# Kernel optimization log

Hardware: AMD Instinct MI355X
Metric: run time of the kernel (lower is better)

## Reference

```python
import jax, jax.numpy as jnp
import numpy as np

TAU = 1.0        # gumbel-softmax temperature
H = 8            # n_heads
RD = 32          # routing_dim


def setup_inputs() -> dict:
    key = jax.random.key(0)
    k1, k2, k3, k4, k5 = jax.random.split(key, 5)
    B, T, C = 2, 2048, 1024
    x = jax.random.normal(k1, (B, T, C), dtype=jnp.float32)
    # base adjacency [H,T,T]; keep diagonal free so each causal row has a finite logit
    base_mask = jax.random.randint(k2, (H, T, T), 0, 2).astype(bool)
    base_mask = base_mask & ~jnp.eye(T, dtype=bool)[None]
    # pre-sampled standard Gumbel noise (matches F.gumbel_softmax internals)
    u = jax.random.uniform(k3, (B, H, T, T), dtype=jnp.float32, minval=1e-9, maxval=1.0)
    gumbel = -jnp.log(-jnp.log(u))
    scale = 1.0 / np.sqrt(C).astype(np.float32)
    Wq = jax.random.normal(k4, (C, H * RD), dtype=jnp.float32) * scale
    Wk = jax.random.normal(k5, (C, H * RD), dtype=jnp.float32) * scale
    return {"x": x, "base_mask": base_mask, "gumbel": gumbel, "Wq": Wq, "Wk": Wk}


def reference(x, base_mask, gumbel, Wq, Wk):
    B, T, C = x.shape
    # routing projections -> [B,T,H,RD]
    sq = (x @ Wq).reshape(B, T, H, RD)
    sk = (x @ Wk).reshape(B, T, H, RD)
    # pairwise edge scores [B,H,T,T]
    scores = jnp.einsum("bihd,bjhd->bhij", sq, sk) / np.sqrt(RD).astype(np.float32)
    # causal mask (j > i) OR already-connected base edges -> -inf
    causal = jnp.triu(jnp.ones((T, T), dtype=bool), 1)
    mask = causal[None, None] | base_mask[None]
    scores = jnp.where(mask, -jnp.inf, scores)
    # gumbel-softmax (training path, hard=False): softmax((logits + g) / tau)
    return jax.nn.softmax((scores + gumbel) / TAU, axis=-1)
```

## Files before the change

kernel.cpp:

```cpp
#include <hip/hip_runtime.h>
#include <hip/hip_bf16.h>
#include <math.h>

#define TT    2048
#define HH    8
#define RDIM  32
#define BB    2

typedef float  f4  __attribute__((ext_vector_type(4)));
typedef int    i4  __attribute__((ext_vector_type(4)));
typedef uint   u2  __attribute__((ext_vector_type(2)));
typedef uint   u4  __attribute__((ext_vector_type(4)));
typedef short  s8v __attribute__((ext_vector_type(8)));

__device__ __forceinline__ uint rnd16(float x) {
    return (__float_as_uint(x) + 0x8000u) >> 16;
}

union v8cast { u4 u; s8v s; };

__global__ __launch_bounds__(256) void wt_prep(
    const float* __restrict__ Wq,
    const float* __restrict__ Wk,
    ushort* __restrict__ Wt)
{
    __shared__ float T[64][68];
    const int k0 = blockIdx.x * 64;
    const int n0 = blockIdx.y * 64;
    const float* W = (n0 < 256) ? Wq : Wk;
    const int nloc = n0 & 255;
    const int tid = threadIdx.x;

    #pragma unroll
    for (int r = 0; r < 4; ++r) {
        int kl  = (tid >> 4) + r * 16;
        int nl4 = (tid & 15) * 4;
        f4 v = *(const f4*)&W[(size_t)(k0 + kl) * 256 + nloc + nl4];
        T[nl4 + 0][kl] = v.x;
        T[nl4 + 1][kl] = v.y;
        T[nl4 + 2][kl] = v.z;
        T[nl4 + 3][kl] = v.w;
    }
    __syncthreads();

    const int nl = tid >> 2;
    const int kq = (tid & 3) * 16;
    u4 o0, o1;
    #pragma unroll
    for (int j = 0; j < 4; ++j) {
        uint lo = rnd16(T[nl][kq + 2 * j]);
        uint hi = rnd16(T[nl][kq + 2 * j + 1]);
        ((uint*)&o0)[j] = (hi << 16) | lo;
    }
    #pragma unroll
    for (int j = 0; j < 4; ++j) {
        uint lo = rnd16(T[nl][kq + 8 + 2 * j]);
        uint hi = rnd16(T[nl][kq + 8 + 2 * j + 1]);
        ((uint*)&o1)[j] = (hi << 16) | lo;
    }
    ushort* dst = Wt + (size_t)(n0 + nl) * 1024 + k0 + kq;
    *(u4*)dst = o0;
    *(u4*)(dst + 8) = o1;
}

__global__ __launch_bounds__(256) void proj_mfma(
    const float* __restrict__ x,
    const ushort* __restrict__ Wt,
    ushort* __restrict__ sqb,
    ushort* __restrict__ skb,
    float* __restrict__ out)
{
    const int tid = threadIdx.x;
    const int l   = tid & 63;
    const int w   = __builtin_amdgcn_readfirstlane(tid) >> 6;
    const int cl  = l & 15;
    const int g4  = l >> 4;
    const int m0  = (blockIdx.x * 4 + w) * 16;
    const int n0  = blockIdx.y * 64;

    f4 acc0 = {0,0,0,0}, acc1 = {0,0,0,0}, acc2 = {0,0,0,0}, acc3 = {0,0,0,0};

    const float*  xrow = x + (size_t)(m0 + cl) * 1024;
    const ushort* wbase = Wt + (size_t)(n0 + cl) * 1024;

    for (int ks = 0; ks < 32; ++ks) {
        const int k = ks * 32 + g4 * 8;
        f4 xa = *(const f4*)&xrow[k];
        f4 xb2 = *(const f4*)&xrow[k + 4];
        v8cast bf;
        ((uint*)&bf.u)[0] = (rnd16(xa.y) << 16) | rnd16(xa.x);
        ((uint*)&bf.u)[1] = (rnd16(xa.w) << 16) | rnd16(xa.z);
        ((uint*)&bf.u)[2] = (rnd16(xb2.y) << 16) | rnd16(xb2.x);
        ((uint*)&bf.u)[3] = (rnd16(xb2.w) << 16) | rnd16(xb2.z);
        s8v a0 = *(const s8v*)(wbase + 0 * 16 * 1024 + k);
        s8v a1 = *(const s8v*)(wbase + 1 * 16 * 1024 + k);
        s8v a2 = *(const s8v*)(wbase + 2 * 16 * 1024 + k);
        s8v a3 = *(const s8v*)(wbase + 3 * 16 * 1024 + k);
        acc0 = __builtin_amdgcn_mfma_f32_16x16x32_bf16(a0, bf.s, acc0, 0, 0, 0);
        acc1 = __builtin_amdgcn_mfma_f32_16x16x32_bf16(a1, bf.s, acc1, 0, 0, 0);
        acc2 = __builtin_amdgcn_mfma_f32_16x16x32_bf16(a2, bf.s, acc2, 0, 0, 0);
        acc3 = __builtin_amdgcn_mfma_f32_16x16x32_bf16(a3, bf.s, acc3, 0, 0, 0);
    }

    const int m = m0 + cl;
    const int nbase = n0 + g4 * 4;
    ushort* obase = (n0 < 256) ? (sqb + (size_t)m * 256 + nbase)
                               : (skb + (size_t)m * 256 + (nbase - 256));
    f4 accs[4] = {acc0, acc1, acc2, acc3};
    #pragma unroll
    for (int t = 0; t < 4; ++t) {
        u2 pk;
        pk.x = (rnd16(accs[t][1]) << 16) | rnd16(accs[t][0]);
        pk.y = (rnd16(accs[t][3]) << 16) | rnd16(accs[t][2]);
        *(u2*)(obase + t * 16) = pk;
    }

    {
        const int zb  = blockIdx.y * 64 + blockIdx.x;
        const int zbh = zb & 15;
        const int sp2 = zb >> 4;
        float* ob = out + (size_t)zbh * TT * TT;
        const int ss[4] = {sp2, 63 - sp2, 64 + sp2, 127 - sp2};
        #pragma unroll
        for (int q = 0; q < 4; ++q) {
            const int s  = ss[q];
            const int i0 = s * 16;
            const int zs = (s + 1) * 16;
            for (int r = 0; r < 16; ++r) {
                float* row = &ob[(size_t)(i0 + r) * TT];
                for (int cz = zs + tid * 4; cz < TT; cz += 256 * 4) {
                    f4 zz = {0.f, 0.f, 0.f, 0.f};
                    *(f4*)&row[cz] = zz;
                }
            }
        }
    }
}

__global__ __launch_bounds__(512) void score_mfma(
    const ushort* __restrict__ sqb,
    const ushort* __restrict__ skb,
    const float*  __restrict__ gumbel,
    const int*    __restrict__ mask,
    float* __restrict__ out)
{
    const int tid = threadIdx.x;
    const int l   = tid & 63;
    const int w   = __builtin_amdgcn_readfirstlane(tid) >> 6;
    const int bh  = blockIdx.x & 15;
    const int sp  = blockIdx.x >> 4;
    const int h   = bh & (HH - 1);
    const int b   = bh >> 3;
    const int cl  = l & 15;
    const int g4  = l >> 4;
    const float RS = 0.17677669529663687f;

    __shared__ float sums_lds[2][8][16];

    const ushort* sqbase = sqb + ((size_t)b * TT) * 256 + h * RDIM + g4 * 8;
    const ushort* skbase = skb + ((size_t)b * TT) * 256 + h * RDIM + g4 * 8;
    const float*  gb = gumbel + (size_t)bh * TT * TT;
    const int*    mb = mask + (size_t)h * TT * TT;
    float*        ob = out + (size_t)bh * TT * TT;

    #pragma unroll 1
    for (int half = 0; half < 2; ++half) {
        const int s      = half ? (127 - sp) : sp;
        const int i0     = s * 16;
        const int ntiles = s + 1;
        const int i      = i0 + cl;

        s8v bfrag = *(const s8v*)(sqbase + (size_t)i * 256);

        const float* grow = gb + (size_t)i * TT;
        const int*   mrow = mb + (size_t)i * TT;
        float*       orow = ob + (size_t)i * TT;

        float sum = 0.f;
        u2 p[8][2];
        #pragma unroll
        for (int it = 0; it < 8; ++it) {
            const int jt0 = 2 * w + it * 16;
            #pragma unroll
            for (int u = 0; u < 2; ++u) {
                const int jt = jt0 + u;
                if (jt < ntiles) {
                    s8v afrag = *(const s8v*)(skbase + (size_t)(jt * 16 + cl) * 256);
                    f4 z = {0.f, 0.f, 0.f, 0.f};
                    f4 c = __builtin_amdgcn_mfma_f32_16x16x32_bf16(
                               afrag, bfrag, z, 0, 0, 0);
                    const int jb = jt * 16 + g4 * 4;
                    f4 gv = *(const f4*)&grow[jb];
                    i4 mv = *(const i4*)&mrow[jb];
                    float e0 = (jb + 0 > i || mv.x) ? 0.f : __expf(fmaf(c[0], RS, gv.x));
                    float e1 = (jb + 1 > i || mv.y) ? 0.f : __expf(fmaf(c[1], RS, gv.y));
                    float e2 = (jb + 2 > i || mv.z) ? 0.f : __expf(fmaf(c[2], RS, gv.z));
                    float e3 = (jb + 3 > i || mv.w) ? 0.f : __expf(fmaf(c[3], RS, gv.w));
                    sum += (e0 + e1) + (e2 + e3);
                    p[it][u].x = (rnd16(e1) << 16) | rnd16(e0);
                    p[it][u].y = (rnd16(e3) << 16) | rnd16(e2);
                }
            }
        }

        sum += __shfl_xor(sum, 16);
        sum += __shfl_xor(sum, 32);
        if (l < 16) sums_lds[half][w][l] = sum;
        __syncthreads();
        float t = 0.f;
        #pragma unroll
        for (int ww = 0; ww < 8; ++ww) t += sums_lds[half][ww][cl];
        const float rinv = 1.0f / t;

        #pragma unroll
        for (int it = 0; it < 8; ++it) {
            const int jt0 = 2 * w + it * 16;
            #pragma unroll
            for (int u = 0; u < 2; ++u) {
                const int jt = jt0 + u;
                if (jt < ntiles) {
                    const int jb = jt * 16 + g4 * 4;
                    f4 v;
                    v.x = __uint_as_float(p[it][u].x << 16) * rinv;
                    v.y = __uint_as_float(p[it][u].x & 0xffff0000u) * rinv;
                    v.z = __uint_as_float(p[it][u].y << 16) * rinv;
                    v.w = __uint_as_float(p[it][u].y & 0xffff0000u) * rinv;
                    *(f4*)&orow[jb] = v;
                }
            }
        }
    }
}

extern "C" void kernel_launch(void* const* d_in, const int* in_sizes, int n_in,
                              void* d_out, int out_size, void* d_ws, size_t ws_size,
                              hipStream_t stream) {
    const float* x      = (const float*)d_in[0];
    const int*   bmask  = (const int*)d_in[1];
    const float* gumbel = (const float*)d_in[2];
    const float* Wq     = (const float*)d_in[3];
    const float* Wk     = (const float*)d_in[4];
    float* out = (float*)d_out;

    ushort* sqb = (ushort*)d_ws;
    ushort* skb = sqb + (size_t)4096 * 256;
    ushort* Wt  = skb + (size_t)4096 * 256;

    wt_prep<<<dim3(16, 8), 256, 0, stream>>>(Wq, Wk, Wt);

    proj_mfma<<<dim3(64, 8), 256, 0, stream>>>(x, Wt, sqb, skb, out);

    score_mfma<<<1024, 512, 0, stream>>>(sqb, skb, gumbel, bmask, out);
}
```

Baseline: 184.1 us.

## Process both batches per block to share base mask loads

Each score block now handles both batch elements for a given head and row-strip, so the int32 base-mask row is loaded once and used for two outputs. The grid is halved to 512 blocks. Batch-1 packed probabilities are staged in LDS to limit register pressure, with an extra barrier per half and launch bounds asking for two blocks per CU. This cuts mask traffic, which is about a fifth of total reads, but halves parallelism and adds LDS use (64KB) that may limit occupancy.

```diff
diff --git a/kernel.cpp b/kernel.cpp
--- a/kernel.cpp
+++ b/kernel.cpp
@@ -137,7 +137,7 @@
     }
 }
 
-__global__ __launch_bounds__(512) void score_mfma(
+__global__ __launch_bounds__(512, 2) void score_mfma(
     const ushort* __restrict__ sqb,
     const ushort* __restrict__ skb,
     const float*  __restrict__ gumbel,
@@ -147,21 +147,24 @@
     const int tid = threadIdx.x;
     const int l   = tid & 63;
     const int w   = __builtin_amdgcn_readfirstlane(tid) >> 6;
-    const int bh  = blockIdx.x & 15;
-    const int sp  = blockIdx.x >> 4;
-    const int h   = bh & (HH - 1);
-    const int b   = bh >> 3;
+    const int h   = blockIdx.x & 7;
+    const int sp  = blockIdx.x >> 3;
     const int cl  = l & 15;
     const int g4  = l >> 4;
     const float RS = 0.17677669529663687f;
 
-    __shared__ float sums_lds[2][8][16];
-
-    const ushort* sqbase = sqb + ((size_t)b * TT) * 256 + h * RDIM + g4 * 8;
-    const ushort* skbase = skb + ((size_t)b * TT) * 256 + h * RDIM + g4 * 8;
-    const float*  gb = gumbel + (size_t)bh * TT * TT;
-    const int*    mb = mask + (size_t)h * TT * TT;
-    float*        ob = out + (size_t)bh * TT * TT;
+    __shared__ u2    p_lds[8][16][64];
+    __shared__ float sums_lds[2][2][8][16];
+
+    const ushort* sqbase0 = sqb + h * RDIM + g4 * 8;
+    const ushort* sqbase1 = sqbase0 + (size_t)TT * 256;
+    const ushort* skbase0 = skb + h * RDIM + g4 * 8;
+    const ushort* skbase1 = skbase0 + (size_t)TT * 256;
+    const float*  gb0 = gumbel + (size_t)h * TT * TT;
+    const float*  gb1 = gb0 + (size_t)HH * TT * TT;
+    const int*    mb  = mask + (size_t)h * TT * TT;
+    float*        ob0 = out + (size_t)h * TT * TT;
+    float*        ob1 = ob0 + (size_t)HH * TT * TT;
 
     #pragma unroll 1
     for (int half = 0; half < 2; ++half) {
@@ -170,14 +173,17 @@
         const int ntiles = s + 1;
         const int i      = i0 + cl;
 
-        s8v bfrag = *(const s8v*)(sqbase + (size_t)i * 256);
-
-        const float* grow = gb + (size_t)i * TT;
-        const int*   mrow = mb + (size_t)i * TT;
-        float*       orow = ob + (size_t)i * TT;
-
-        float sum = 0.f;
-        u2 p[8][2];
+        s8v bfrag0 = *(const s8v*)(sqbase0 + (size_t)i * 256);
+        s8v bfrag1 = *(const s8v*)(sqbase1 + (size_t)i * 256);
+
+        const float* grow0 = gb0 + (size_t)i * TT;
+        const float* grow1 = gb1 + (size_t)i * TT;
+        const int*   mrow  = mb  + (size_t)i * TT;
+        float*       orow0 = ob0 + (size_t)i * TT;
+        float*       orow1 = ob1 + (size_t)i * TT;
+
+        float sum0 = 0.f, sum1 = 0.f;
+        u2 p0[8][2];
         #pragma unroll
         for (int it = 0; it < 8; ++it) {
             const int jt0 = 2 * w + it * 16;
@@ -185,32 +191,55 @@
             for (int u = 0; u < 2; ++u) {
                 const int jt = jt0 + u;
                 if (jt < ntiles) {
-                    s8v afrag = *(const s8v*)(skbase + (size_t)(jt * 16 + cl) * 256);
+                    const size_t arow = (size_t)(jt * 16 + cl) * 256;
+                    s8v af0 = *(const s8v*)(skbase0 + arow);
+                    s8v af1 = *(const s8v*)(skbase1 + arow);
+                    const int jb = jt * 16 + g4 * 4;
+                    i4 mv = *(const i4*)&mrow[jb];
+                    f4 gv0 = *(const f4*)&grow0[jb];
+                    f4 gv1 = *(const f4*)&grow1[jb];
                     f4 z = {0.f, 0.f, 0.f, 0.f};
-                    f4 c = __builtin_amdgcn_mfma_f32_16x16x32_bf16(
-                               afrag, bfrag, z, 0, 0, 0);
-                    const int jb = jt * 16 + g4 * 4;
-                    f4 gv = *(const f4*)&grow[jb];
-                    i4 mv = *(const i4*)&mrow[jb];
-                    float e0 = (jb + 0 > i || mv.x) ? 0.f : __expf(fmaf(c[0], RS, gv.x));
-                    float e1 = (jb + 1 > i || mv.y) ? 0.f : __expf(fmaf(c[1], RS, gv.y));
-                    float e2 = (jb + 2 > i || mv.z) ? 0.f : __expf(fmaf(c[2], RS, gv.z));
-                    float e3 = (jb + 3 > i || mv.w) ? 0.f : __expf(fmaf(c[3], RS, gv.w));
-                    sum += (e0 + e1) + (e2 + e3);
-                    p[it][u].x = (rnd16(e1) << 16) | rnd16(e0);
-                    p[it][u].y = (rnd16(e3) << 16) | rnd16(e2);
+                    f4 c0 = __builtin_amdgcn_mfma_f32_16x16x32_bf16(
+                                af0, bfrag0, z, 0, 0, 0);
+                    f4 c1 = __builtin_amdgcn_mfma_f32_16x16x32_bf16(
+                                af1, bfrag1, z, 0, 0, 0);
+                    float e00 = (jb + 0 > i || mv.x) ? 0.f : __expf(fmaf(c0[0], RS, gv0.x));
+                    float e01 = (jb + 1 > i || mv.y) ? 0.f : __expf(fmaf(c0[1], RS, gv0.y));
+                    float e02 = (jb + 2 > i || mv.z) ? 0.f : __expf(fmaf(c0[2], RS, gv0.z));
+                    float e03 = (jb + 3 > i || mv.w) ? 0.f : __expf(fmaf(c0[3], RS, gv0.w));
+                    float e10 = (jb + 0 > i || mv.x) ? 0.f : __expf(fmaf(c1[0], RS, gv1.x));
+                    float e11 = (jb + 1 > i || mv.y) ? 0.f : __expf(fmaf(c1[1], RS, gv1.y));
+                    float e12 = (jb + 2 > i || mv.z) ? 0.f : __expf(fmaf(c1[2], RS, gv1.z));
+                    float e13 = (jb + 3 > i || mv.w) ? 0.f : __expf(fmaf(c1[3], RS, gv1.w));
+                    sum0 += (e00 + e01) + (e02 + e03);
+                    sum1 += (e10 + e11) + (e12 + e13);
+                    p0[it][u].x = (rnd16(e01) << 16) | rnd16(e00);
+                    p0[it][u].y = (rnd16(e03) << 16) | rnd16(e02);
+                    u2 pk1;
+                    pk1.x = (rnd16(e11) << 16) | rnd16(e10);
+                    pk1.y = (rnd16(e13) << 16) | rnd16(e12);
+                    p_lds[w][it * 2 + u][l] = pk1;
                 }
             }
         }
 
-        sum += __shfl_xor(sum, 16);
-        sum += __shfl_xor(sum, 32);
-        if (l < 16) sums_lds[half][w][l] = sum;
+        sum0 += __shfl_xor(sum0, 16);
+        sum0 += __shfl_xor(sum0, 32);
+        sum1 += __shfl_xor(sum1, 16);
+        sum1 += __shfl_xor(sum1, 32);
+        if (l < 16) {
+            sums_lds[half][0][w][l] = sum0;
+            sums_lds[half][1][w][l] = sum1;
+        }
         __syncthreads();
-        float t = 0.f;
-        #pragma unroll
-        for (int ww = 0; ww < 8; ++ww) t += sums_lds[half][ww][cl];
-        const float rinv = 1.0f / t;
+        float t0 = 0.f, t1 = 0.f;
+        #pragma unroll
+        for (int ww = 0; ww < 8; ++ww) {
+            t0 += sums_lds[half][0][ww][cl];
+            t1 += sums_lds[half][1][ww][cl];
+        }
+        const float rinv0 = 1.0f / t0;
+        const float rinv1 = 1.0f / t1;
 
         #pragma unroll
         for (int it = 0; it < 8; ++it) {
@@ -220,15 +249,23 @@
                 const int jt = jt0 + u;
                 if (jt < ntiles) {
                     const int jb = jt * 16 + g4 * 4;
-                    f4 v;
-                    v.x = __uint_as_float(p[it][u].x << 16) * rinv;
-                    v.y = __uint_as_float(p[it][u].x & 0xffff0000u) * rinv;
-                    v.z = __uint_as_float(p[it][u].y << 16) * rinv;
-                    v.w = __uint_as_float(p[it][u].y & 0xffff0000u) * rinv;
-                    *(f4*)&orow[jb] = v;
+                    f4 v0;
+                    v0.x = __uint_as_float(p0[it][u].x << 16) * rinv0;
+                    v0.y = __uint_as_float(p0[it][u].x & 0xffff0000u) * rinv0;
+                    v0.z = __uint_as_float(p0[it][u].y << 16) * rinv0;
+                    v0.w = __uint_as_float(p0[it][u].y & 0xffff0000u) * rinv0;
+                    *(f4*)&orow0[jb] = v0;
+                    u2 pk1 = p_lds[w][it * 2 + u][l];
+                    f4 v1;
+                    v1.x = __uint_as_float(pk1.x << 16) * rinv1;
+                    v1.y = __uint_as_float(pk1.x & 0xffff0000u) * rinv1;
+                    v1.z = __uint_as_float(pk1.y << 16) * rinv1;
+                    v1.w = __uint_as_float(pk1.y & 0xffff0000u) * rinv1;
+                    *(f4*)&orow1[jb] = v1;
                 }
             }
         }
+        __syncthreads();
     }
 }
 
@@ -250,5 +287,5 @@
 
     proj_mfma<<<dim3(64, 8), 256, 0, stream>>>(x, Wt, sqb, skb, out);
 
-    score_mfma<<<1024, 512, 0, stream>>>(sqb, skb, gumbel, bmask, out);
-}
+    score_mfma<<<512, 512, 0, stream>>>(sqb, skb, gumbel, bmask, out);
+}
```

New measurement: 185.5 us. No clear change (+0.8%).
